# Kernel tuning notes

Measured on AMD Instinct MI355X. Metric: run time of the kernel, lower is better.

## Reference

```python
import jax, jax.numpy as jnp
import numpy as np

B, H, V, NS, S, D, E = 4096, 256, 32000, 2, 128, 4, 64
PAD = 0


def _shift_matrices(n):
    # W_up: row i <- row i+1, last row zero. W_down: row i <- row i-1, row 0 zero.
    eye = np.eye(n, dtype=np.float32)
    W_up = np.vstack([eye[1:], np.zeros((1, n), np.float32)])
    W_down = np.vstack([np.zeros((1, n), np.float32), eye[:-1]])
    return W_up, W_down


def setup_inputs() -> dict:
    key = jax.random.key(0)
    ks = jax.random.split(key, 20)
    sc = 0.05
    emb_table = jax.random.normal(ks[0], (V, H), jnp.float32) * sc
    emb_table = emb_table.at[PAD].set(0.0)  # padding_idx
    inp = {
        "input_ids": jax.random.randint(ks[1], (B,), 0, V),
        "hidden": jax.random.normal(ks[2], (B, H), jnp.float32),
        "stacks": jax.random.normal(ks[3], (B, NS, S, E), jnp.float32),
        "emb_table": emb_table,
        "W_in": jax.random.normal(ks[4], (H, H), jnp.float32) * sc,
        "b_in": jnp.zeros((H,), jnp.float32),
        "W_hh": jax.random.normal(ks[5], (H, H), jnp.float32) * sc,
        "b_hh": jnp.zeros((H,), jnp.float32),
        "W_s2h": jax.random.normal(ks[6], (NS, H, D * E), jnp.float32) * sc,
        "b_s2h": jnp.zeros((NS, H), jnp.float32),
        "W_act": jax.random.normal(ks[7], (NS, 3, H), jnp.float32) * sc,
        "b_act": jnp.zeros((NS, 3), jnp.float32),
        "W_push": jax.random.normal(ks[8], (NS, E, H), jnp.float32) * sc,
        "b_push": jnp.zeros((NS, E), jnp.float32),
        "W_out": jax.random.normal(ks[9], (V, H), jnp.float32) * sc,
        "b_out": jnp.zeros((V,), jnp.float32),
        "empty_elem": jax.random.normal(ks[10], (1, E), jnp.float32),
    }
    return inp


def reference(input_ids, hidden, stacks, emb_table, W_in, b_in, W_hh, b_hh,
              W_s2h, b_s2h, W_act, b_act, W_push, b_push, W_out, b_out,
              empty_elem):
    W_up_np, W_down_np = _shift_matrices(S)
    W_up = jnp.asarray(W_up_np)
    W_down = jnp.asarray(W_down_np)

    emb = emb_table[input_ids]                                  # [B,H]
    mid = emb @ W_in.T + b_in + hidden @ W_hh.T + b_hh          # [B,H]

    # stack readout (top stack_depth elems), before any update
    stack_vals = stacks[:, :, :D, :].reshape(B, NS, D * E)      # [B,NS,D*E]
    mid = mid + jnp.einsum('bnd,nhd->bh', stack_vals, W_s2h) + b_s2h.sum(0)

    # per-stack actions from the OLD hidden state (no softmax in source)
    act = jnp.einsum('bh,nah->bna', hidden, W_act) + b_act      # [B,NS,3]
    p_push = act[..., 0:1]                                      # [B,NS,1]
    p_pop = act[..., 1:2]
    p_noop = act[..., 2:3]
    push_val = jnp.tanh(jnp.einsum('bh,neh->bne', hidden, W_push) + b_push)  # [B,NS,E]

    down = jnp.einsum('st,bnte->bnse', W_down, stacks)          # shift down
    up = jnp.einsum('st,bnte->bnse', W_up, stacks)              # shift up
    new_stacks = (p_push[..., None] * down + p_pop[..., None] * up
                  + p_noop[..., None] * stacks)
    new_stacks = new_stacks.at[:, :, 0, :].set(p_push * push_val)
    new_stacks = new_stacks.at[:, :, S - 1, :].set(
        jnp.broadcast_to(empty_elem[None], (B, NS, E)))

    new_hidden = jnp.tanh(mid)                                  # [B,H]
    logits = new_hidden @ W_out.T + b_out                       # [B,V]
    output = jax.nn.log_softmax(logits, axis=1)
    top1 = jnp.argmax(output, axis=1)[:, None]                  # [B,1]
    return output, new_hidden, top1, new_stacks
```

## Files before the change

### kernel.cpp

```cpp
#include <hip/hip_runtime.h>
#include <stdint.h>

#define B_   4096
#define H_   256
#define V_   32000
#define NS_  2
#define S_   128
#define E_   64
#define TRIG 0.02f
#define CSTR 10
#define NTV  125

typedef __attribute__((ext_vector_type(4))) float  f32x4;
typedef __attribute__((ext_vector_type(8))) __bf16 bf16x8;

__device__ __forceinline__ unsigned short f2bf(float f) {
  unsigned u = __float_as_uint(f);
  u += 0x7fffu + ((u >> 16) & 1u);
  return (unsigned short)(u >> 16);
}

typedef __attribute__((address_space(1))) const unsigned int* gas1_t;
typedef __attribute__((address_space(3))) unsigned int*       las3_t;
__device__ __forceinline__ void gload16(const void* g, void* l) {
  __builtin_amdgcn_global_load_lds((gas1_t)g, (las3_t)l, 16, 0, 0);
}

__device__ __forceinline__ void merge2(float& m1, float& i1, float& m2, float& i2,
                                       float om1, float oi1, float om2, float oi2) {
  if (om1 > m1 || (om1 == m1 && oi1 < i1)) {
    const float lm = m1, li = i1;
    m1 = om1; i1 = oi1;
    if (lm > om2 || (lm == om2 && li < oi2)) { m2 = lm; i2 = li; }
    else { m2 = om2; i2 = oi2; }
  } else {
    if (om1 > m2 || (om1 == m2 && oi1 < i2)) { m2 = om1; i2 = oi1; }
  }
}

__global__ void prep_w1(const float* __restrict__ W_in,  const float* __restrict__ W_hh,
                        const float* __restrict__ W_s2h, const float* __restrict__ W_act,
                        const float* __restrict__ W_push,
                        const float* __restrict__ b_in,  const float* __restrict__ b_hh,
                        const float* __restrict__ b_s2h, const float* __restrict__ b_act,
                        const float* __restrict__ b_push,
                        unsigned short* __restrict__ W1, float* __restrict__ bbig) {
  const unsigned idx = blockIdx.x * 256u + threadIdx.x;
  const unsigned c = idx >> 10, k = idx & 1023u;
  float w = 0.f;
  if (c < 256u) {
    if (k < 256u)       w = W_in[c*256u + k];
    else if (k < 512u)  w = W_hh[c*256u + (k-256u)];
    else { unsigned n = (k-512u) >> 8, d = (k-512u) & 255u; w = W_s2h[n*65536u + c*256u + d]; }
  } else if (c < 262u) {
    if (k >= 256u && k < 512u) w = W_act[(c-256u)*256u + (k-256u)];
  } else if (c < 390u) {
    if (k >= 256u && k < 512u) w = W_push[(c-262u)*256u + (k-256u)];
  }
  W1[(size_t)c*1024u + k] = f2bf(w);
  if (idx < 512u) {
    float bb = 0.f;
    if (idx < 256u)       bb = b_in[idx] + b_hh[idx] + b_s2h[idx] + b_s2h[256u+idx];
    else if (idx < 262u)  bb = b_act[idx-256u];
    else if (idx < 390u)  bb = b_push[idx-262u];
    bbig[idx] = bb;
  }
}

__global__ void prep_w1t(const float* __restrict__ W_in, const float* __restrict__ W_hh,
                         const float* __restrict__ W_s2h, float* __restrict__ W1T) {
  const unsigned idx = blockIdx.x * 256u + threadIdx.x;
  const unsigned k = idx >> 8, h = idx & 255u;
  float w;
  if (k < 256u)      w = W_in[h*256u + k];
  else if (k < 512u) w = W_hh[h*256u + (k-256u)];
  else { unsigned n = (k-512u) >> 8, d = (k-512u) & 255u; w = W_s2h[n*65536u + h*256u + d]; }
  W1T[idx] = w;
}

__global__ void prep_a1(const int* __restrict__ ids, const float* __restrict__ emb,
                        const float* __restrict__ hidden, const float* __restrict__ stacks,
                        unsigned short* __restrict__ A1, float* __restrict__ A1f) {
  const unsigned idx = blockIdx.x * 256u + threadIdx.x;
  const unsigned b = idx >> 10, k = idx & 1023u;
  float x;
  if (k < 256u)      x = emb[(size_t)ids[b]*256u + k];
  else if (k < 512u) x = hidden[(size_t)b*256u + (k-256u)];
  else { unsigned kk = k - 512u, n = kk >> 8, f = kk & 255u;
         x = stacks[(size_t)b*16384u + n*8192u + f]; }
  A1[(size_t)b*1024u + k] = f2bf(x);
  A1f[(size_t)b*1024u + k] = x;
}

__global__ void prep_b2(const float* __restrict__ W_out, unsigned short* __restrict__ B2) {
  const unsigned idx = blockIdx.x * 256u + threadIdx.x;
  B2[idx] = f2bf(W_out[idx]);
}

__global__ __launch_bounds__(256) void gemm_mid(
    const unsigned short* __restrict__ A, const unsigned short* __restrict__ Bm,
    float* __restrict__ nh_out, float* __restrict__ actw, float* __restrict__ pushw,
    const float* __restrict__ bbig, unsigned short* __restrict__ a2w)
{
  constexpr int K = 1024;
  constexpr int NT = K >> 6;
  __shared__ __align__(16) unsigned char pool[65536];
  const int tid  = threadIdx.x;
  const int lane = tid & 63;
  const int wid  = tid >> 6;
  const int wm = wid >> 1, wn = wid & 1;
  const int l16 = lane & 15;
  const int lk8 = (lane >> 4) << 3;
  const int lr4 = (lane >> 4) << 2;
  const size_t arow0 = (size_t)blockIdx.y << 7;
  const size_t bcol0 = (size_t)blockIdx.x << 7;

  f32x4 acc[4][4];
#pragma unroll
  for (int i = 0; i < 4; ++i)
#pragma unroll
    for (int j = 0; j < 4; ++j) acc[i][j] = (f32x4)0.f;

  auto stageAB = [&](int buf, int kt) {
    unsigned char* dst = pool + (buf << 15);
    const int k0 = kt << 6;
#pragma unroll
    for (int i = 0; i < 4; ++i) {
      const int e   = (i << 8) + tid;
      const int row = e >> 3;
      const int col = (e & 7) << 3;
      gload16(A  + (arow0 + row) * (size_t)K + (k0 + col), dst + (size_t)e * 16);
      gload16(Bm + (bcol0 + row) * (size_t)K + (k0 + col), dst + 16384 + (size_t)e * 16);
    }
  };
  auto computeT = [&](int buf) {
    const unsigned short* As = (const unsigned short*)(pool + (buf << 15));
    const unsigned short* Bs = As + 8192;
#pragma unroll
    for (int kk = 0; kk < 64; kk += 32) {
      bf16x8 af[4], bfr[4];
#pragma unroll
      for (int f = 0; f < 4; ++f) {
        af[f]  = *(const bf16x8*)&As[((wm<<6) + (f<<4) + l16)*64 + kk + lk8];
        bfr[f] = *(const bf16x8*)&Bs[((wn<<6) + (f<<4) + l16)*64 + kk + lk8];
      }
#pragma unroll
      for (int mf = 0; mf < 4; ++mf)
#pragma unroll
        for (int nf = 0; nf < 4; ++nf)
          acc[mf][nf] = __builtin_amdgcn_mfma_f32_16x16x32_bf16(af[mf], bfr[nf], acc[mf][nf], 0, 0, 0);
    }
  };

  stageAB(0, 0);
  __syncthreads();
  int cur = 0;
#pragma unroll
  for (int t = 0; t < NT - 1; ++t) {
    stageAB(cur ^ 1, t + 1);
    computeT(cur);
    __syncthreads();
    cur ^= 1;
  }
  computeT(cur);

#pragma unroll
  for (int mf = 0; mf < 4; ++mf)
#pragma unroll
    for (int j = 0; j < 4; ++j) {
      const int r = (int)arow0 + (wm<<6) + (mf<<4) + lr4 + j;
#pragma unroll
      for (int nf = 0; nf < 4; ++nf) {
        const int c = (int)bcol0 + (wn<<6) + (nf<<4) + l16;
        const float v = acc[mf][nf][j] + bbig[c];
        if (c < 256) { const float th = tanhf(v);
                       nh_out[r*256 + c] = th;
                       a2w[r*256 + c] = f2bf(th); }
        else if (c < 262)  actw[r*6 + (c-256)] = v;
        else if (c < 390)  pushw[r*128 + (c-262)] = tanhf(v);
      }
    }
}

template<int MODE>
__global__ __launch_bounds__(512, 2) void gemm256(
    const unsigned short* __restrict__ Am, const unsigned short* __restrict__ Bn,
    float* __restrict__ gout, const float* __restrict__ b_out,
    float* __restrict__ partials, const float* __restrict__ subw)
{
  __shared__ __align__(16) unsigned char pool[66560];
  const int tid  = threadIdx.x;
  const int lane = tid & 63;
  const int wid  = tid >> 6;
  const int wm = wid >> 2;
  const int wn = wid & 3;
  const int l16 = lane & 15;
  const int g4  = lane >> 4;
  const int lk8 = g4 << 3;
  const int lr4 = g4 << 2;

  const int lin = ((int)blockIdx.x & 7) * 250 + ((int)blockIdx.x >> 3);
  const int bty = lin & 15;
  const int btx = lin >> 4;
  const size_t m0 = (size_t)(MODE == 0 ? bty : btx) << 8;
  const size_t n0 = (size_t)(MODE == 0 ? btx : bty) << 8;

  f32x4 acc[8][4];
#pragma unroll
  for (int m = 0; m < 8; ++m)
#pragma unroll
    for (int n = 0; n < 4; ++n) acc[m][n] = (f32x4)0.f;

  auto stage = [&](int buf, int ks) {
    unsigned char* da = pool + (buf << 15);
    unsigned char* db = da + 16384;
    const int k0 = ks << 5;
#pragma unroll
    for (int i = 0; i < 2; ++i) {
      const int e   = (i << 9) + tid;
      const int row = e >> 2;
      const int c16 = (e & 3) << 3;
      gload16(Am + (m0 + row) * 256 + k0 + c16, da + (size_t)e * 16);
      gload16(Bn + (n0 + row) * 256 + k0 + c16, db + (size_t)e * 16);
    }
  };
  auto compute = [&](int buf) {
    const unsigned short* As = (const unsigned short*)(pool + (buf << 15));
    const unsigned short* Bs = As + 8192;
    bf16x8 af[8], bfr[4];
#pragma unroll
    for (int m = 0; m < 8; ++m)
      af[m] = *(const bf16x8*)&As[((wm<<7) + (m<<4) + l16)*32 + lk8];
#pragma unroll
    for (int n = 0; n < 4; ++n)
      bfr[n] = *(const bf16x8*)&Bs[((wn<<6) + (n<<4) + l16)*32 + lk8];
#pragma unroll
    for (int m = 0; m < 8; ++m)
#pragma unroll
      for (int n = 0; n < 4; ++n)
        acc[m][n] = __builtin_amdgcn_mfma_f32_16x16x32_bf16(af[m], bfr[n], acc[m][n], 0, 0, 0);
  };

  stage(0, 0);
  __syncthreads();
  int cur = 0;
#pragma unroll
  for (int t = 0; t < 7; ++t) {
    stage(cur ^ 1, t + 1);
    compute(cur);
    __syncthreads();
    cur ^= 1;
  }
  compute(cur);

  if constexpr (MODE == 0) {
    float* lf = (float*)pool;
#pragma unroll
    for (int ch = 0; ch < 4; ++ch) {
      __syncthreads();
      if (wm == (ch >> 1)) {
        const int mh = ch & 1;
#pragma unroll
        for (int mi = 0; mi < 4; ++mi) {
          const int m = mh*4 + mi;
#pragma unroll
          for (int n = 0; n < 4; ++n) {
            const int col = (wn<<6) + (n<<4) + l16;
#pragma unroll
            for (int j = 0; j < 4; ++j)
              lf[(mi*16 + lr4 + j)*260 + col] = acc[m][n][j];
          }
        }
      }
      __syncthreads();
      const int rbase = (ch >> 1)*128 + (ch & 1)*64;
#pragma unroll
      for (int it = 0; it < 8; ++it) {
        const int e  = (it << 9) + tid;
        const int r  = e >> 6;
        const int c4 = (e & 63) << 2;
        float4 v = *(float4*)&lf[r*260 + c4];
        const float4 bo4 = *(const float4*)&b_out[n0 + c4];
        const size_t grow = m0 + rbase + r;
        const float ls = subw[grow];
        v.x += bo4.x - ls; v.y += bo4.y - ls; v.z += bo4.z - ls; v.w += bo4.w - ls;
        *(float4*)&gout[grow * (size_t)V_ + n0 + c4] = v;
      }
    }
  } else {
    float (*colrec)[5] = (float (*)[5])&pool[0];
    float bo[32];
#pragma unroll
    for (int m = 0; m < 8; ++m)
#pragma unroll
      for (int j = 0; j < 4; ++j)
        bo[m*4+j] = b_out[m0 + (wm<<7) + (m<<4) + lr4 + j];

    float rS[4], rM1[4], rI1[4], rM2[4], rI2[4];
#pragma unroll
    for (int n = 0; n < 4; ++n) {
      float s = 0.f, m1 = -INFINITY, i1f = 2.1e9f, m2 = -INFINITY, i2f = 2.1e9f;
#pragma unroll
      for (int m = 0; m < 8; ++m)
#pragma unroll
        for (int j = 0; j < 4; ++j) {
          const int vloc = (wm<<7) + (m<<4) + lr4 + j;
          const float v = acc[m][n][j] + bo[m*4+j];
          const float fi = (float)((int)m0 + vloc);
          s += __expf(v);
          if (v > m1 || (v == m1 && fi < i1f)) { m2 = m1; i2f = i1f; m1 = v; i1f = fi; }
          else if (v > m2 || (v == m2 && fi < i2f)) { m2 = v; i2f = fi; }
        }
#pragma unroll
      for (int mask = 16; mask <= 32; mask <<= 1) {
        const float os  = __shfl_xor(s,   mask, 64);
        const float om1 = __shfl_xor(m1,  mask, 64);
        const float oi1 = __shfl_xor(i1f, mask, 64);
        const float om2 = __shfl_xor(m2,  mask, 64);
        const float oi2 = __shfl_xor(i2f, mask, 64);
        s += os;
        merge2(m1, i1f, m2, i2f, om1, oi1, om2, oi2);
      }
      rS[n] = s; rM1[n] = m1; rI1[n] = i1f; rM2[n] = m2; rI2[n] = i2f;
    }
    if (wm == 0 && g4 == 0) {
#pragma unroll
      for (int n = 0; n < 4; ++n) {
        const int cl = (wn<<6) + (n<<4) + l16;
        colrec[cl][0] = rS[n];  colrec[cl][1] = rM1[n]; colrec[cl][2] = rI1[n];
        colrec[cl][3] = rM2[n]; colrec[cl][4] = rI2[n];
      }
    }
    __syncthreads();
    if (wm == 1 && g4 == 0) {
#pragma unroll
      for (int n = 0; n < 4; ++n) {
        const int cl = (wn<<6) + (n<<4) + l16;
        float s = rS[n] + colrec[cl][0];
        float m1 = rM1[n], i1f = rI1[n], m2 = rM2[n], i2f = rI2[n];
        merge2(m1, i1f, m2, i2f, colrec[cl][1], colrec[cl][2], colrec[cl][3], colrec[cl][4]);
        const size_t brow = n0 + cl;
        float* dst = partials + (brow * NTV + btx) * 8;
        float4 v4; v4.x = s; v4.y = m1; v4.z = i1f; v4.w = m2;
        *(float4*)dst = v4;
        dst[4] = i2f;
      }
    }
  }
}

__global__ __launch_bounds__(256) void reduce_kernel(
    const float* __restrict__ partials, float* __restrict__ subw,
    float* __restrict__ top1w, int* __restrict__ candbuf)
{
  const int b = blockIdx.x, t = threadIdx.x;
  float s = 0.f, m1 = -INFINITY, i1 = 2.1e9f, m2 = -INFINITY, i2 = 2.1e9f;
  if (t < NTV) {
    const float4 p0 = *(const float4*)(partials + ((size_t)b*NTV + t)*8);
    s = p0.x; m1 = p0.y; i1 = p0.z; m2 = p0.w;
    i2 = partials[((size_t)b*NTV + t)*8 + 4];
  }
  __shared__ float sS[256], sM1[256], sI1[256], sM2[256], sI2[256];
  sS[t] = s; sM1[t] = m1; sI1[t] = i1; sM2[t] = m2; sI2[t] = i2;
  __syncthreads();
  for (int off = 128; off > 0; off >>= 1) {
    if (t < off) {
      sS[t] += sS[t+off];
      float a1 = sM1[t], ai1 = sI1[t], a2 = sM2[t], ai2 = sI2[t];
      merge2(a1, ai1, a2, ai2, sM1[t+off], sI1[t+off], sM2[t+off], sI2[t+off]);
      sM1[t] = a1; sI1[t] = ai1; sM2[t] = a2; sI2[t] = ai2;
    }
    __syncthreads();
  }
  const float M1 = sM1[0];
  __shared__ int cnt; __shared__ int cand[CSTR-1];
  if (t == 0) cnt = 0;
  __syncthreads();
  if (t < NTV) {
    if (m1 >= M1 - TRIG) { int p = atomicAdd(&cnt, 1); if (p < CSTR-1) cand[p] = (int)i1; }
    if (m2 >= M1 - TRIG) { int p = atomicAdd(&cnt, 1); if (p < CSTR-1) cand[p] = (int)i2; }
  }
  __syncthreads();
  const int ncand = min(cnt, CSTR-1);
  if (t == 0) {
    subw[b] = logf(sS[0]);
    candbuf[b*CSTR] = ncand;
    if (ncand <= 1) top1w[b] = sI1[0];
  }
  if (t < ncand) candbuf[b*CSTR + 1 + t] = cand[t];
}

__global__ __launch_bounds__(256) void rescue_kernel(
    const int* __restrict__ candbuf, const float* __restrict__ A1f,
    const float* __restrict__ W1T, const float* __restrict__ bbig,
    const float* __restrict__ W_out, const float* __restrict__ b_out,
    float* __restrict__ top1w)
{
  const int b = blockIdx.x;
  const int ncand = candbuf[b*CSTR];
  if (ncand <= 1) return;
  const int t = threadIdx.x;

  double acc = (double)bbig[t];
  const float* arow = A1f + (size_t)b * 1024;
  for (int k = 0; k < 1024; ++k)
    acc += (double)arow[k] * (double)W1T[k*256 + t];
  __shared__ double hbuf[256];
  hbuf[t] = tanh(acc);
  __syncthreads();

  __shared__ double red[256];
  double best = -1e300; int besti = 0x7fffffff;
  for (int q = 0; q < ncand; ++q) {
    const int ci = candbuf[b*CSTR + 1 + q];
    red[t] = hbuf[t] * (double)W_out[(size_t)ci*256 + t];
    __syncthreads();
    for (int off = 128; off > 0; off >>= 1) {
      if (t < off) red[t] += red[t+off];
      __syncthreads();
    }
    if (t == 0) {
      const double d = red[0] + (double)b_out[ci];
      if (d > best || (d == best && ci < besti)) { best = d; besti = ci; }
    }
    __syncthreads();
  }
  if (t == 0) top1w[b] = (float)besti;
}

__global__ void stacks_kernel(const float* __restrict__ stacks, const float* __restrict__ actw,
                              const float* __restrict__ pushw, const float* __restrict__ empty,
                              float* __restrict__ out3) {
  const int bn = blockIdx.x;
  const int b = bn >> 1, n = bn & 1;
  __shared__ __align__(16) float st[S_*E_];
  const float4* src4 = (const float4*)(stacks + (size_t)bn * (S_*E_));
  float4* st4 = (float4*)st;
  for (int i = threadIdx.x; i < (S_*E_/4); i += 256) st4[i] = src4[i];
  __syncthreads();
  const float pp = actw[b*6 + n*3 + 0];
  const float po = actw[b*6 + n*3 + 1];
  const float pq = actw[b*6 + n*3 + 2];
  float4* dst4 = (float4*)(out3 + (size_t)bn * (S_*E_));
  for (int i = threadIdx.x; i < (S_*E_/4); i += 256) {
    const int flat = i << 2;
    const int s = flat >> 6;
    const int e = flat & 63;
    float4 r;
    if (s == S_-1) {
      r = ((const float4*)empty)[e >> 2];
    } else if (s == 0) {
      const float4 pv = ((const float4*)(pushw + b*128 + n*64))[e >> 2];
      r.x = pp*pv.x; r.y = pp*pv.y; r.z = pp*pv.z; r.w = pp*pv.w;
    } else {
      const float4 dn = *(const float4*)&st[(s-1)*64 + e];
      const float4 up = *(const float4*)&st[(s+1)*64 + e];
      const float4 cu = *(const float4*)&st[s*64 + e];
      r.x = pp*dn.x + po*up.x + pq*cu.x;
      r.y = pp*dn.y + po*up.y + pq*cu.y;
      r.z = pp*dn.z + po*up.z + pq*cu.z;
      r.w = pp*dn.w + po*up.w + pq*cu.w;
    }
    dst4[i] = r;
  }
}

extern "C" void kernel_launch(void* const* d_in, const int* in_sizes, int n_in,
                              void* d_out, int out_size, void* d_ws, size_t ws_size,
                              hipStream_t stream) {
  (void)in_sizes; (void)n_in; (void)out_size; (void)ws_size;
  const int*   ids    = (const int*)  d_in[0];
  const float* hidden = (const float*)d_in[1];
  const float* stacks = (const float*)d_in[2];
  const float* emb    = (const float*)d_in[3];
  const float* W_in   = (const float*)d_in[4];
  const float* b_in   = (const float*)d_in[5];
  const float* W_hh   = (const float*)d_in[6];
  const float* b_hh   = (const float*)d_in[7];
  const float* W_s2h  = (const float*)d_in[8];
  const float* b_s2h  = (const float*)d_in[9];
  const float* W_act  = (const float*)d_in[10];
  const float* b_act  = (const float*)d_in[11];
  const float* W_push = (const float*)d_in[12];
  const float* b_push = (const float*)d_in[13];
  const float* W_out  = (const float*)d_in[14];
  const float* b_out  = (const float*)d_in[15];
  const float* empty  = (const float*)d_in[16];

  float* out0 = (float*)d_out;
  float* out1 = out0 + (size_t)B_*V_;
  float* out2 = out1 + (size_t)B_*H_;
  float* out3 = out2 + B_;

  unsigned short* A1 = (unsigned short*)out3;
  unsigned short* W1 = A1 + (size_t)4194304;
  unsigned short* A2 = W1 + (size_t)524288;
  unsigned short* B2 = A2 + (size_t)1048576;
  float* partials    = (float*)(B2 + (size_t)8192000);
  float* A1f         = partials + (size_t)8192000;
  float* W1T         = A1f + (size_t)4194304;
  int*   candbuf     = (int*)(W1T + 262144);

  float* bbig  = (float*)d_ws;
  float* actw  = bbig + 512;
  float* pushw = actw + (size_t)B_*6;
  float* subw  = pushw + (size_t)B_*128;

  prep_w1<<<dim3(2048),  dim3(256), 0, stream>>>(W_in, W_hh, W_s2h, W_act, W_push,
                                                 b_in, b_hh, b_s2h, b_act, b_push, W1, bbig);
  prep_w1t<<<dim3(1024), dim3(256), 0, stream>>>(W_in, W_hh, W_s2h, W1T);
  prep_a1<<<dim3(16384), dim3(256), 0, stream>>>(ids, emb, hidden, stacks, A1, A1f);
  gemm_mid<<<dim3(4, 32), dim3(256), 0, stream>>>(A1, W1, out1, actw, pushw, bbig, A2);
  prep_b2<<<dim3(32000), dim3(256), 0, stream>>>(W_out, B2);
  gemm256<2><<<dim3(2000), dim3(512), 0, stream>>>(B2, A2,
      nullptr, b_out, partials, nullptr);
  reduce_kernel<<<dim3(4096), dim3(256), 0, stream>>>(partials, subw, out2, candbuf);
  gemm256<0><<<dim3(2000), dim3(512), 0, stream>>>(A2, B2,
      out0, b_out, nullptr, subw);
  rescue_kernel<<<dim3(4096), dim3(256), 0, stream>>>(candbuf, A1f, W1T, bbig,
                                                      W_out, b_out, out2);
  stacks_kernel<<<dim3(8192), dim3(256), 0, stream>>>(stacks, actw, pushw, empty, out3);
}
```

Measured before the change: 657.4 us.

## Vectorize prep kernels and deepen GEMM pipelines with swizzled 64-wide K tiles

The prep_a1 and prep_b2 conversion kernels now handle 8 elements per thread using float4 loads and 16-byte bf16 stores, with launch grids shrunk to match. gemm256 moves to 64-wide K tiles in a 128KB LDS double buffer with an XOR swizzle to avoid bank conflicts. Both gemm256 and gemm_mid replace __syncthreads with explicit vmcnt waits and raw barriers so that two stages are in flight. The larger LDS footprint lowers occupancy under launch_bounds(512,2), and the hand-written vmcnt counts must match the number of outstanding loads per stage.

```diff
diff --git a/kernel.cpp b/kernel.cpp
--- a/kernel.cpp
+++ b/kernel.cpp
@@ -13,6 +13,7 @@
 
 typedef __attribute__((ext_vector_type(4))) float  f32x4;
 typedef __attribute__((ext_vector_type(8))) __bf16 bf16x8;
+typedef __attribute__((ext_vector_type(8))) unsigned short u16x8;
 
 __device__ __forceinline__ unsigned short f2bf(float f) {
   unsigned u = __float_as_uint(f);
@@ -81,20 +82,32 @@
 __global__ void prep_a1(const int* __restrict__ ids, const float* __restrict__ emb,
                         const float* __restrict__ hidden, const float* __restrict__ stacks,
                         unsigned short* __restrict__ A1, float* __restrict__ A1f) {
-  const unsigned idx = blockIdx.x * 256u + threadIdx.x;
-  const unsigned b = idx >> 10, k = idx & 1023u;
-  float x;
-  if (k < 256u)      x = emb[(size_t)ids[b]*256u + k];
-  else if (k < 512u) x = hidden[(size_t)b*256u + (k-256u)];
-  else { unsigned kk = k - 512u, n = kk >> 8, f = kk & 255u;
-         x = stacks[(size_t)b*16384u + n*8192u + f]; }
-  A1[(size_t)b*1024u + k] = f2bf(x);
-  A1f[(size_t)b*1024u + k] = x;
+  const unsigned gid = blockIdx.x * 256u + threadIdx.x;
+  const unsigned b = gid >> 7, k0 = (gid & 127u) << 3;
+  const float* src;
+  if (k0 < 256u)      src = emb + (size_t)ids[b]*256u + k0;
+  else if (k0 < 512u) src = hidden + (size_t)b*256u + (k0-256u);
+  else { const unsigned kk = k0 - 512u;
+         src = stacks + (size_t)b*16384u + (kk>>8)*8192u + (kk&255u); }
+  const float4 v0 = *(const float4*)src;
+  const float4 v1 = *(const float4*)(src + 4);
+  *(float4*)(A1f + (size_t)b*1024u + k0)     = v0;
+  *(float4*)(A1f + (size_t)b*1024u + k0 + 4) = v1;
+  u16x8 o;
+  o[0]=f2bf(v0.x); o[1]=f2bf(v0.y); o[2]=f2bf(v0.z); o[3]=f2bf(v0.w);
+  o[4]=f2bf(v1.x); o[5]=f2bf(v1.y); o[6]=f2bf(v1.z); o[7]=f2bf(v1.w);
+  *(u16x8*)(A1 + (size_t)b*1024u + k0) = o;
 }
 
 __global__ void prep_b2(const float* __restrict__ W_out, unsigned short* __restrict__ B2) {
-  const unsigned idx = blockIdx.x * 256u + threadIdx.x;
-  B2[idx] = f2bf(W_out[idx]);
+  const unsigned gid = blockIdx.x * 256u + threadIdx.x;
+  const size_t base = (size_t)gid * 8;
+  const float4 v0 = *(const float4*)(W_out + base);
+  const float4 v1 = *(const float4*)(W_out + base + 4);
+  u16x8 o;
+  o[0]=f2bf(v0.x); o[1]=f2bf(v0.y); o[2]=f2bf(v0.z); o[3]=f2bf(v0.w);
+  o[4]=f2bf(v1.x); o[5]=f2bf(v1.y); o[6]=f2bf(v1.z); o[7]=f2bf(v1.w);
+  *(u16x8*)(B2 + base) = o;
 }
 
 __global__ __launch_bounds__(256) void gemm_mid(
@@ -153,16 +166,16 @@
   };
 
   stageAB(0, 0);
-  __syncthreads();
-  int cur = 0;
-#pragma unroll
-  for (int t = 0; t < NT - 1; ++t) {
-    stageAB(cur ^ 1, t + 1);
-    computeT(cur);
-    __syncthreads();
-    cur ^= 1;
-  }
-  computeT(cur);
+  stageAB(1, 1);
+#pragma unroll
+  for (int t = 0; t < NT; ++t) {
+    if (t < NT - 1) asm volatile("s_waitcnt vmcnt(8)" ::: "memory");
+    else            asm volatile("s_waitcnt vmcnt(0)" ::: "memory");
+    __builtin_amdgcn_s_barrier();
+    computeT(t & 1);
+    __builtin_amdgcn_s_barrier();
+    if (t + 2 < NT) stageAB(t & 1, t + 2);
+  }
 
 #pragma unroll
   for (int mf = 0; mf < 4; ++mf)
@@ -188,7 +201,7 @@
     float* __restrict__ gout, const float* __restrict__ b_out,
     float* __restrict__ partials, const float* __restrict__ subw)
 {
-  __shared__ __align__(16) unsigned char pool[66560];
+  __shared__ __align__(16) unsigned char pool[131072];
   const int tid  = threadIdx.x;
   const int lane = tid & 63;
   const int wid  = tid >> 6;
@@ -196,7 +209,6 @@
   const int wn = wid & 3;
   const int l16 = lane & 15;
   const int g4  = lane >> 4;
-  const int lk8 = g4 << 3;
   const int lr4 = g4 << 2;
 
   const int lin = ((int)blockIdx.x & 7) * 250 + ((int)blockIdx.x >> 3);
@@ -212,46 +224,54 @@
     for (int n = 0; n < 4; ++n) acc[m][n] = (f32x4)0.f;
 
   auto stage = [&](int buf, int ks) {
-    unsigned char* da = pool + (buf << 15);
-    unsigned char* db = da + 16384;
-    const int k0 = ks << 5;
-#pragma unroll
-    for (int i = 0; i < 2; ++i) {
+    unsigned char* da = pool + (buf ? 65536 : 0);
+    unsigned char* db = da + 32768;
+    const int k0 = ks << 6;
+#pragma unroll
+    for (int i = 0; i < 4; ++i) {
       const int e   = (i << 9) + tid;
-      const int row = e >> 2;
-      const int c16 = (e & 3) << 3;
-      gload16(Am + (m0 + row) * 256 + k0 + c16, da + (size_t)e * 16);
-      gload16(Bn + (n0 + row) * 256 + k0 + c16, db + (size_t)e * 16);
+      const int row = e >> 3;
+      const int ch  = (e & 7) ^ (row & 7);
+      gload16(Am + (m0 + row) * 256 + k0 + (ch << 3), da + (size_t)e * 16);
+      gload16(Bn + (n0 + row) * 256 + k0 + (ch << 3), db + (size_t)e * 16);
     }
   };
   auto compute = [&](int buf) {
-    const unsigned short* As = (const unsigned short*)(pool + (buf << 15));
-    const unsigned short* Bs = As + 8192;
-    bf16x8 af[8], bfr[4];
-#pragma unroll
-    for (int m = 0; m < 8; ++m)
-      af[m] = *(const bf16x8*)&As[((wm<<7) + (m<<4) + l16)*32 + lk8];
-#pragma unroll
-    for (int n = 0; n < 4; ++n)
-      bfr[n] = *(const bf16x8*)&Bs[((wn<<6) + (n<<4) + l16)*32 + lk8];
-#pragma unroll
-    for (int m = 0; m < 8; ++m)
-#pragma unroll
-      for (int n = 0; n < 4; ++n)
-        acc[m][n] = __builtin_amdgcn_mfma_f32_16x16x32_bf16(af[m], bfr[n], acc[m][n], 0, 0, 0);
+    const unsigned short* As = (const unsigned short*)(pool + (buf ? 65536 : 0));
+    const unsigned short* Bs = As + 16384;
+#pragma unroll
+    for (int kk = 0; kk < 64; kk += 32) {
+      const int cb = (kk >> 3) + g4;
+      bf16x8 af[8], bfr[4];
+#pragma unroll
+      for (int m = 0; m < 8; ++m) {
+        const int row = (wm<<7) + (m<<4) + l16;
+        af[m] = *(const bf16x8*)&As[row*64 + ((cb ^ (row & 7)) << 3)];
+      }
+#pragma unroll
+      for (int n = 0; n < 4; ++n) {
+        const int row = (wn<<6) + (n<<4) + l16;
+        bfr[n] = *(const bf16x8*)&Bs[row*64 + ((cb ^ (row & 7)) << 3)];
+      }
+#pragma unroll
+      for (int m = 0; m < 8; ++m)
+#pragma unroll
+        for (int n = 0; n < 4; ++n)
+          acc[m][n] = __builtin_amdgcn_mfma_f32_16x16x32_bf16(af[m], bfr[n], acc[m][n], 0, 0, 0);
+    }
   };
 
   stage(0, 0);
-  __syncthreads();
-  int cur = 0;
-#pragma unroll
-  for (int t = 0; t < 7; ++t) {
-    stage(cur ^ 1, t + 1);
-    compute(cur);
-    __syncthreads();
-    cur ^= 1;
-  }
-  compute(cur);
+  stage(1, 1);
+#pragma unroll
+  for (int t = 0; t < 4; ++t) {
+    if (t < 3) asm volatile("s_waitcnt vmcnt(8)" ::: "memory");
+    else       asm volatile("s_waitcnt vmcnt(0)" ::: "memory");
+    __builtin_amdgcn_s_barrier();
+    compute(t & 1);
+    __builtin_amdgcn_s_barrier();
+    if (t < 2) stage(t & 1, t + 2);
+  }
 
   if constexpr (MODE == 0) {
     float* lf = (float*)pool;
@@ -509,9 +529,9 @@
   prep_w1<<<dim3(2048),  dim3(256), 0, stream>>>(W_in, W_hh, W_s2h, W_act, W_push,
                                                  b_in, b_hh, b_s2h, b_act, b_push, W1, bbig);
   prep_w1t<<<dim3(1024), dim3(256), 0, stream>>>(W_in, W_hh, W_s2h, W1T);
-  prep_a1<<<dim3(16384), dim3(256), 0, stream>>>(ids, emb, hidden, stacks, A1, A1f);
+  prep_a1<<<dim3(2048),  dim3(256), 0, stream>>>(ids, emb, hidden, stacks, A1, A1f);
   gemm_mid<<<dim3(4, 32), dim3(256), 0, stream>>>(A1, W1, out1, actw, pushw, bbig, A2);
-  prep_b2<<<dim3(32000), dim3(256), 0, stream>>>(W_out, B2);
+  prep_b2<<<dim3(4000),  dim3(256), 0, stream>>>(W_out, B2);
   gemm256<2><<<dim3(2000), dim3(512), 0, stream>>>(B2, A2,
       nullptr, b_out, partials, nullptr);
   reduce_kernel<<<dim3(4096), dim3(256), 0, stream>>>(partials, subw, out2, candbuf);
```

Result: faster. 637.6 us (-3.0%).
